# Kernel optimization log

Measured on AMD Instinct MI355X. Metric: run time of the kernel, lower is better.

The kernel has to match this reference:

```python
import jax, jax.numpy as jnp
import numpy as np


def setup_inputs() -> dict:
    key = jax.random.key(0)
    k_x, k0, k1, k2, kb = jax.random.split(key, 5)
    D, C, KH, KW = 256, 128, 3, 3
    R1, R2 = 8, 4
    x = jax.random.normal(k_x, (32, C, 64, 64), dtype=jnp.float32)
    # TT cores (leading/trailing rank-1 dims squeezed), init U(-0.77, 0.77) as in the torch module
    core0 = jax.random.uniform(k0, (D, C, R1), dtype=jnp.float32, minval=-0.77, maxval=0.77)
    core1 = jax.random.uniform(k1, (D, R1, KH, R2), dtype=jnp.float32, minval=-0.77, maxval=0.77)
    core2 = jax.random.uniform(k2, (D, R2, KW), dtype=jnp.float32, minval=-0.77, maxval=0.77)
    bias = jax.random.uniform(kb, (1,), dtype=jnp.float32, minval=-0.1, maxval=0.1)
    return {"x": x, "core0": core0, "core1": core1, "core2": core2,
            "bias": bias, "stride": 1, "pad": 1}


def reference(x, core0, core1, core2, bias, stride, pad):
    # Reconstruct the full conv kernel from the TT cores: [D, C, kH, kW]
    kernel = jnp.einsum('dcr,drks,dsj->dckj', core0, core1, core2)
    # Same math as pad + unfold + einsum('nchwkj,dckj->ndhw'): a standard cross-correlation conv
    out = jax.lax.conv_general_dilated(
        x, kernel,
        window_strides=(stride, stride),
        padding=[(pad, pad), (pad, pad)],
        dimension_numbers=('NCHW', 'OIHW', 'NCHW'))
    # scalar bias broadcast over all output channels (bias.view(1,-1,1,1) with 1 element)
    return out + bias.reshape(1, -1, 1, 1)
```

## Files before the change

kernel.cpp:

```cpp
#include <hip/hip_runtime.h>

typedef __bf16 bf16x8 __attribute__((ext_vector_type(8)));
typedef float f32x4 __attribute__((ext_vector_type(4)));

__device__ __forceinline__ unsigned short f2bf(float f) {
    union { float f; unsigned int u; } v; v.f = f;
    unsigned int u = v.u;
    unsigned int r = (u + 0x7fffu + ((u >> 16) & 1u)) >> 16;
    return (unsigned short)r;
}

__global__ void build_w_kernel(const float* __restrict__ core0,
                               const float* __restrict__ core1,
                               const float* __restrict__ core2,
                               unsigned short* __restrict__ wb) {
    __shared__ float s1[96];
    __shared__ float s2[12];
    const int d = blockIdx.x;
    const int c = threadIdx.x;
    if (c < 96) s1[c] = core1[d * 96 + c];
    if (c >= 96 && c < 108) s2[c - 96] = core2[d * 12 + (c - 96)];
    __syncthreads();
    float t0[8];
#pragma unroll
    for (int r = 0; r < 8; ++r) t0[r] = core0[(d * 128 + c) * 8 + r];
#pragma unroll
    for (int kh = 0; kh < 3; ++kh) {
        float v[4] = {0.f, 0.f, 0.f, 0.f};
#pragma unroll
        for (int r = 0; r < 8; ++r)
#pragma unroll
            for (int s = 0; s < 4; ++s)
                v[s] += t0[r] * s1[(r * 3 + kh) * 4 + s];
#pragma unroll
        for (int kw = 0; kw < 3; ++kw) {
            float val = 0.f;
#pragma unroll
            for (int s = 0; s < 4; ++s) val += v[s] * s2[s * 3 + kw];
            const int kidx = (kh * 3 + kw) * 128 + c;
            wb[(kidx >> 3) * 2048 + d * 8 + (kidx & 7)] = f2bf(val);
        }
    }
}

#define LC 136

__global__ __launch_bounds__(256) void conv_mfma_kernel(
    const float* __restrict__ x, const unsigned short* __restrict__ wb,
    const float* __restrict__ bias, float* __restrict__ out) {
    __shared__ __align__(16) unsigned short xl[3 * 66 * LC];
    __shared__ __align__(16) unsigned short bl[32 * 256];

    const int tid  = threadIdx.x;
    const int lane = tid & 63;
    const int wv   = tid >> 6;
    const int l15  = lane & 15;
    const int quad = lane >> 4;
    const int bid  = blockIdx.x;
    const int n    = bid >> 6;
    const int h    = bid & 63;

    uint4* xz = (uint4*)xl;
    const uint4 z4 = make_uint4(0u, 0u, 0u, 0u);
    for (int i = tid; i < (3 * 66 * LC * 2) / 16; i += 256) xz[i] = z4;
    __syncthreads();

#pragma unroll
    for (int i = 0; i < 6; ++i) {
        const int it  = tid + (i << 8);
        const int w4  = it & 15;
        const int cg  = (it >> 4) & 31;
        const int row = it >> 9;
        const int rimg = h + row - 1;
        if (rimg >= 0 && rimg < 64) {
            const int c = cg << 2;
            const int w = w4 << 2;
            const float4* gp = (const float4*)(x + (((n * 128 + c) * 64 + rimg) * 64 + w));
            const float4 p0 = gp[0];
            const float4 p1 = gp[1024];
            const float4 p2 = gp[2048];
            const float4 p3 = gp[3072];
            unsigned short* base = xl + (row * 66 + w + 1) * LC + c;
            *(ushort4*)(base)           = make_ushort4(f2bf(p0.x), f2bf(p1.x), f2bf(p2.x), f2bf(p3.x));
            *(ushort4*)(base + LC)      = make_ushort4(f2bf(p0.y), f2bf(p1.y), f2bf(p2.y), f2bf(p3.y));
            *(ushort4*)(base + 2 * LC)  = make_ushort4(f2bf(p0.z), f2bf(p1.z), f2bf(p2.z), f2bf(p3.z));
            *(ushort4*)(base + 3 * LC)  = make_ushort4(f2bf(p0.w), f2bf(p1.w), f2bf(p2.w), f2bf(p3.w));
        }
    }

    f32x4 acc[4][4];
#pragma unroll
    for (int a0 = 0; a0 < 4; ++a0)
#pragma unroll
        for (int b0 = 0; b0 < 4; ++b0) acc[a0][b0] = (f32x4){0.f, 0.f, 0.f, 0.f};

    const uint4* wg = (const uint4*)wb;
    uint4 rw0 = wg[tid], rw1 = wg[tid + 256], rw2 = wg[tid + 512], rw3 = wg[tid + 768];

    const int dwave = wv << 6;
    uint4* blv = (uint4*)bl;

    for (int ch = 0; ch < 36; ++ch) {
        __syncthreads();
        blv[tid]       = rw0;
        blv[tid + 256] = rw1;
        blv[tid + 512] = rw2;
        blv[tid + 768] = rw3;
        __syncthreads();
        if (ch + 1 < 36) {
            const uint4* g2 = wg + (ch + 1) * 1024;
            rw0 = g2[tid]; rw1 = g2[tid + 256]; rw2 = g2[tid + 512]; rw3 = g2[tid + 768];
        }
        const int tap = ch >> 2;
        const int kh  = tap / 3;
        const int kw  = tap - kh * 3;
        const int c0  = (ch & 3) << 5;

        bf16x8 af[4], bfr[4];
        const unsigned short* ap = bl + (quad * 256 + dwave + l15) * 8;
#pragma unroll
        for (int dt = 0; dt < 4; ++dt) af[dt] = *(const bf16x8*)(ap + dt * 128);
        const unsigned short* bp = xl + (kh * 66 + l15 + kw) * LC + c0 + quad * 8;
#pragma unroll
        for (int pt = 0; pt < 4; ++pt) bfr[pt] = *(const bf16x8*)(bp + pt * 16 * LC);

#pragma unroll
        for (int dt = 0; dt < 4; ++dt)
#pragma unroll
            for (int pt = 0; pt < 4; ++pt)
                acc[dt][pt] = __builtin_amdgcn_mfma_f32_16x16x32_bf16(
                    af[dt], bfr[pt], acc[dt][pt], 0, 0, 0);
    }

    const float bv = bias[0];
#pragma unroll
    for (int dt = 0; dt < 4; ++dt) {
#pragma unroll
        for (int pt = 0; pt < 4; ++pt) {
#pragma unroll
            for (int r = 0; r < 4; ++r) {
                const int d = dwave + dt * 16 + quad * 4 + r;
                const int w = pt * 16 + l15;
                out[((n * 256 + d) * 64 + h) * 64 + w] = acc[dt][pt][r] + bv;
            }
        }
    }
}

extern "C" void kernel_launch(void* const* d_in, const int* in_sizes, int n_in,
                              void* d_out, int out_size, void* d_ws, size_t ws_size,
                              hipStream_t stream) {
    const float* x     = (const float*)d_in[0];
    const float* core0 = (const float*)d_in[1];
    const float* core1 = (const float*)d_in[2];
    const float* core2 = (const float*)d_in[3];
    const float* bias  = (const float*)d_in[4];
    unsigned short* wb = (unsigned short*)d_ws;

    build_w_kernel<<<256, 128, 0, stream>>>(core0, core1, core2, wb);
    conv_mfma_kernel<<<2048, 256, 0, stream>>>(x, wb, bias, (float*)d_out);
}
```

Before: 288.6 us.

## Load weight fragments directly from global into registers, drop LDS staging and barriers

The weight operand is no longer staged through shared memory each chunk with two barriers per iteration. Each lane now loads its MFMA A-fragments straight from global (L2-resident) memory, with a one-chunk register prefetch. The full LDS zero-fill is replaced by zeroing only the halo columns and writing zeros for out-of-range rows, and launch bounds request 3 blocks per CU. This removes barrier stalls and LDS traffic and frees shared memory for occupancy, at the cost of more global/L2 load traffic per wave and higher register pressure.

```diff
diff --git a/kernel.cpp b/kernel.cpp
--- a/kernel.cpp
+++ b/kernel.cpp
@@ -45,11 +45,10 @@
 
 #define LC 136
 
-__global__ __launch_bounds__(256) void conv_mfma_kernel(
+__global__ __launch_bounds__(256, 3) void conv_mfma_kernel(
     const float* __restrict__ x, const unsigned short* __restrict__ wb,
     const float* __restrict__ bias, float* __restrict__ out) {
     __shared__ __align__(16) unsigned short xl[3 * 66 * LC];
-    __shared__ __align__(16) unsigned short bl[32 * 256];
 
     const int tid  = threadIdx.x;
     const int lane = tid & 63;
@@ -60,33 +59,38 @@
     const int n    = bid >> 6;
     const int h    = bid & 63;
 
-    uint4* xz = (uint4*)xl;
-    const uint4 z4 = make_uint4(0u, 0u, 0u, 0u);
-    for (int i = tid; i < (3 * 66 * LC * 2) / 16; i += 256) xz[i] = z4;
-    __syncthreads();
+    if (tid < 96) {
+        const int row = tid >> 5;
+        const int j   = tid & 31;
+        const int col = (j >> 4) ? 65 : 0;
+        const int c   = (j & 15) << 3;
+        *(uint4*)(xl + (row * 66 + col) * LC + c) = make_uint4(0u, 0u, 0u, 0u);
+    }
 
-#pragma unroll
+#pragma unroll 2
     for (int i = 0; i < 6; ++i) {
         const int it  = tid + (i << 8);
         const int w4  = it & 15;
         const int cg  = (it >> 4) & 31;
         const int row = it >> 9;
         const int rimg = h + row - 1;
+        float4 p0 = make_float4(0.f, 0.f, 0.f, 0.f), p1 = p0, p2 = p0, p3 = p0;
+        const int c = cg << 2;
+        const int w = w4 << 2;
         if (rimg >= 0 && rimg < 64) {
-            const int c = cg << 2;
-            const int w = w4 << 2;
             const float4* gp = (const float4*)(x + (((n * 128 + c) * 64 + rimg) * 64 + w));
-            const float4 p0 = gp[0];
-            const float4 p1 = gp[1024];
-            const float4 p2 = gp[2048];
-            const float4 p3 = gp[3072];
-            unsigned short* base = xl + (row * 66 + w + 1) * LC + c;
-            *(ushort4*)(base)           = make_ushort4(f2bf(p0.x), f2bf(p1.x), f2bf(p2.x), f2bf(p3.x));
-            *(ushort4*)(base + LC)      = make_ushort4(f2bf(p0.y), f2bf(p1.y), f2bf(p2.y), f2bf(p3.y));
-            *(ushort4*)(base + 2 * LC)  = make_ushort4(f2bf(p0.z), f2bf(p1.z), f2bf(p2.z), f2bf(p3.z));
-            *(ushort4*)(base + 3 * LC)  = make_ushort4(f2bf(p0.w), f2bf(p1.w), f2bf(p2.w), f2bf(p3.w));
+            p0 = gp[0];
+            p1 = gp[1024];
+            p2 = gp[2048];
+            p3 = gp[3072];
         }
+        unsigned short* base = xl + (row * 66 + w + 1) * LC + c;
+        *(ushort4*)(base)          = make_ushort4(f2bf(p0.x), f2bf(p1.x), f2bf(p2.x), f2bf(p3.x));
+        *(ushort4*)(base + LC)     = make_ushort4(f2bf(p0.y), f2bf(p1.y), f2bf(p2.y), f2bf(p3.y));
+        *(ushort4*)(base + 2 * LC) = make_ushort4(f2bf(p0.z), f2bf(p1.z), f2bf(p2.z), f2bf(p3.z));
+        *(ushort4*)(base + 3 * LC) = make_ushort4(f2bf(p0.w), f2bf(p1.w), f2bf(p2.w), f2bf(p3.w));
     }
+    __syncthreads();
 
     f32x4 acc[4][4];
 #pragma unroll
@@ -94,42 +98,43 @@
 #pragma unroll
         for (int b0 = 0; b0 < 4; ++b0) acc[a0][b0] = (f32x4){0.f, 0.f, 0.f, 0.f};
 
-    const uint4* wg = (const uint4*)wb;
-    uint4 rw0 = wg[tid], rw1 = wg[tid + 256], rw2 = wg[tid + 512], rw3 = wg[tid + 768];
+    const int dwave = wv << 6;
+    const bf16x8* wgv = (const bf16x8*)wb;
+    const int abase = quad * 256 + dwave + l15;
 
-    const int dwave = wv << 6;
-    uint4* blv = (uint4*)bl;
+    bf16x8 an[4];
+#pragma unroll
+    for (int dt = 0; dt < 4; ++dt) an[dt] = wgv[abase + dt * 16];
 
-    for (int ch = 0; ch < 36; ++ch) {
-        __syncthreads();
-        blv[tid]       = rw0;
-        blv[tid + 256] = rw1;
-        blv[tid + 512] = rw2;
-        blv[tid + 768] = rw3;
-        __syncthreads();
-        if (ch + 1 < 36) {
-            const uint4* g2 = wg + (ch + 1) * 1024;
-            rw0 = g2[tid]; rw1 = g2[tid + 256]; rw2 = g2[tid + 512]; rw3 = g2[tid + 768];
-        }
-        const int tap = ch >> 2;
-        const int kh  = tap / 3;
-        const int kw  = tap - kh * 3;
-        const int c0  = (ch & 3) << 5;
-
-        bf16x8 af[4], bfr[4];
-        const unsigned short* ap = bl + (quad * 256 + dwave + l15) * 8;
-#pragma unroll
-        for (int dt = 0; dt < 4; ++dt) af[dt] = *(const bf16x8*)(ap + dt * 128);
-        const unsigned short* bp = xl + (kh * 66 + l15 + kw) * LC + c0 + quad * 8;
-#pragma unroll
-        for (int pt = 0; pt < 4; ++pt) bfr[pt] = *(const bf16x8*)(bp + pt * 16 * LC);
+    const unsigned short* bb = xl + l15 * LC + quad * 8;
 
 #pragma unroll
-        for (int dt = 0; dt < 4; ++dt)
+    for (int tap = 0; tap < 9; ++tap) {
+        const int kh = tap / 3;
+        const int kw = tap - kh * 3;
 #pragma unroll
-            for (int pt = 0; pt < 4; ++pt)
-                acc[dt][pt] = __builtin_amdgcn_mfma_f32_16x16x32_bf16(
-                    af[dt], bfr[pt], acc[dt][pt], 0, 0, 0);
+        for (int c4 = 0; c4 < 4; ++c4) {
+            const int ch = tap * 4 + c4;
+            bf16x8 ac[4];
+#pragma unroll
+            for (int dt = 0; dt < 4; ++dt) ac[dt] = an[dt];
+            if (ch + 1 < 36) {
+                const bf16x8* g2 = wgv + (ch + 1) * 1024 + abase;
+#pragma unroll
+                for (int dt = 0; dt < 4; ++dt) an[dt] = g2[dt * 16];
+            }
+            const int c0 = c4 << 5;
+            bf16x8 bfr[4];
+            const unsigned short* bp = bb + (kh * 66 + kw) * LC + c0;
+#pragma unroll
+            for (int pt = 0; pt < 4; ++pt) bfr[pt] = *(const bf16x8*)(bp + pt * 16 * LC);
+#pragma unroll
+            for (int dt = 0; dt < 4; ++dt)
+#pragma unroll
+                for (int pt = 0; pt < 4; ++pt)
+                    acc[dt][pt] = __builtin_amdgcn_mfma_f32_16x16x32_bf16(
+                        ac[dt], bfr[pt], acc[dt][pt], 0, 0, 0);
+        }
     }
 
     const float bv = bias[0];
```

Result: faster. 248.8 us (-13.8%).
